# Optimization experiments

Hardware: AMD Instinct MI355X
Metric: run time of the kernel (lower is better)

The kernel has to match this reference:

```python
import jax, jax.numpy as jnp
import numpy as np

WS = 7      # window size
NH = 8      # num heads

def setup_inputs() -> dict:
    key = jax.random.key(0)
    k1, k2, k3 = jax.random.split(key, 3)
    B, H, W, C = 32, 56, 56, 256
    x = jax.random.normal(k1, (B, H, W, C), dtype=jnp.float32)
    w_qkv = jax.random.normal(k2, (3 * C, C), dtype=jnp.float32) * 0.02
    w_proj = jax.random.normal(k3, (C, C), dtype=jnp.float32) * 0.02
    b_proj = jnp.zeros((C,), dtype=jnp.float32)
    return {"x": x, "w_qkv": w_qkv, "w_proj": w_proj, "b_proj": b_proj}

def reference(x, w_qkv, w_proj, b_proj):
    B, H, W, C = x.shape
    hd = C // NH
    scale = hd ** -0.5
    # window partition: (B,H,W,C) -> (nW, ws^2, C)
    xw = x.reshape(B, H // WS, WS, W // WS, WS, C)
    xw = xw.transpose(0, 1, 3, 2, 4, 5).reshape(-1, WS * WS, C)
    # fused qkv projection (no bias)
    qkv = (xw @ w_qkv.T).reshape(-1, WS * WS, 3, NH, hd)
    q, k, v = qkv[:, :, 0], qkv[:, :, 1], qkv[:, :, 2]  # (nW, ws^2, nh, hd)
    # NOTE: faithful to source quirk — contraction over head_dim per token,
    # producing an (nh x nh) head-mixing attention matrix per token.
    attn = jnp.einsum('nshd,nsed->nshe', q, k) * scale   # (nW, ws^2, nh, nh)
    attn = jax.nn.softmax(attn, axis=-1)
    out = jnp.einsum('nshe,nsed->nshd', attn, v)         # (nW, ws^2, nh, hd)
    # source does transpose(1,2).reshape(-1, ws^2, C) — replicate exactly
    out = out.swapaxes(1, 2).reshape(-1, WS * WS, C)
    out = out @ w_proj.T + b_proj
    # window un-partition
    out = out.reshape(B, H // WS, W // WS, WS, WS, C)
    out = out.transpose(0, 1, 3, 2, 4, 5).reshape(B, H, W, C)
    return out
```

## Files before the change

### kernel.cpp

```cpp
#include <hip/hip_runtime.h>
#include <hip/hip_bf16.h>

typedef __bf16 bf16_t;
typedef bf16_t bf16x8 __attribute__((ext_vector_type(8)));
typedef float floatx4 __attribute__((ext_vector_type(4)));

__global__ __launch_bounds__(256) void wconv_kernel(
    const float* __restrict__ w_qkv, const float* __restrict__ w_proj,
    bf16_t* __restrict__ wb)
{
  int idx4 = (blockIdx.x * 256 + threadIdx.x) * 4;
  const float* src = (idx4 < 196608) ? (w_qkv + idx4) : (w_proj + (idx4 - 196608));
  float4 f = *(const float4*)src;
  bf16_t o[4] = {(bf16_t)f.x, (bf16_t)f.y, (bf16_t)f.z, (bf16_t)f.w};
  *(uint2*)(wb + idx4) = *(const uint2*)o;
}

__global__ __launch_bounds__(512, 4) void fused_kernel(
    const float* __restrict__ x,
    const bf16_t* __restrict__ wb,
    const float* __restrict__ b_proj,
    float* __restrict__ out)
{
  __shared__ __align__(16) bf16_t Xs[49][264];
  __shared__ __align__(16) bf16_t KV[49][264];
  __shared__ __align__(16) bf16_t Qt[49][72];
  __shared__ _Float16 Pl[49][64];
  __shared__ int trow[49];

  const int n = blockIdx.x;
  const int b = n >> 6, wh = (n >> 3) & 7, ww = n & 7;
  const int tid = threadIdx.x;
  const int wave = tid >> 6, lane = tid & 63, quad = lane >> 4, l16 = lane & 15;
  const float scale = 0.17677669529663687f;

  if (tid < 49) {
    int i = tid / 7, j = tid % 7;
    trow[tid] = b * 3136 + (wh * 7 + i) * 56 + ww * 7 + j;
  }
  __syncthreads();

  for (int idx = tid; idx < 49 * 32; idx += 512) {
    int s = idx >> 5, g = (idx & 31) * 8;
    const float* p = x + (long)trow[s] * 256 + g;
    float4 f0 = ((const float4*)p)[0];
    float4 f1 = ((const float4*)p)[1];
    bf16_t t8[8] = {(bf16_t)f0.x, (bf16_t)f0.y, (bf16_t)f0.z, (bf16_t)f0.w,
                    (bf16_t)f1.x, (bf16_t)f1.y, (bf16_t)f1.z, (bf16_t)f1.w};
    *(uint4*)(&Xs[s][g]) = *(const uint4*)t8;
  }
  __syncthreads();

  {
    floatx4 acc[4][2] = {};
    const int cb = wave * 32;
    const bf16_t* wk = wb + (256 + cb) * 256;
#pragma unroll
    for (int k = 0; k < 8; ++k) {
      bf16x8 a[4], bfr[2];
#pragma unroll
      for (int i = 0; i < 4; ++i) {
        int mr = i * 16 + l16; if (mr > 48) mr = 48;
        a[i] = *(const bf16x8*)(&Xs[mr][k * 32 + quad * 8]);
      }
#pragma unroll
      for (int j = 0; j < 2; ++j)
        bfr[j] = *(const bf16x8*)(wk + (j * 16 + l16) * 256 + k * 32 + quad * 8);
#pragma unroll
      for (int i = 0; i < 4; ++i)
#pragma unroll
        for (int j = 0; j < 2; ++j)
          acc[i][j] = __builtin_amdgcn_mfma_f32_16x16x32_bf16(a[i], bfr[j], acc[i][j], 0, 0, 0);
    }
#pragma unroll
    for (int i = 0; i < 4; ++i)
#pragma unroll
      for (int r = 0; r < 4; ++r) {
        int m = i * 16 + quad * 4 + r;
        if (m < 49) {
#pragma unroll
          for (int j = 0; j < 2; ++j)
            KV[m][cb + j * 16 + l16] = (bf16_t)acc[i][j][r];
        }
      }
  }
  __syncthreads();

  for (int hp = 0; hp < 4; ++hp) {
    const int jw = wave & 3;
    const int ih = wave >> 2;
    floatx4 qacc[2] = {};
    const bf16_t* wq = wb + (hp * 64 + jw * 16) * 256;
#pragma unroll
    for (int k = 0; k < 8; ++k) {
      bf16x8 a[2];
#pragma unroll
      for (int ii = 0; ii < 2; ++ii) {
        int mr = (ih * 2 + ii) * 16 + l16; if (mr > 48) mr = 48;
        a[ii] = *(const bf16x8*)(&Xs[mr][k * 32 + quad * 8]);
      }
      bf16x8 bfr = *(const bf16x8*)(wq + l16 * 256 + k * 32 + quad * 8);
#pragma unroll
      for (int ii = 0; ii < 2; ++ii)
        qacc[ii] = __builtin_amdgcn_mfma_f32_16x16x32_bf16(a[ii], bfr, qacc[ii], 0, 0, 0);
    }
#pragma unroll
    for (int ii = 0; ii < 2; ++ii)
#pragma unroll
      for (int r = 0; r < 4; ++r) {
        int m = (ih * 2 + ii) * 16 + quad * 4 + r;
        if (m < 49) Qt[m][jw * 16 + l16] = (bf16_t)qacc[ii][r];
      }
    __syncthreads();

    if (tid < 98) {
      int s = tid >> 1, hl = tid & 1;
      float qf[32];
#pragma unroll
      for (int u = 0; u < 4; ++u) {
        bf16x8 qv = *(const bf16x8*)(&Qt[s][hl * 32 + u * 8]);
#pragma unroll
        for (int d = 0; d < 8; ++d) qf[u * 8 + d] = (float)qv[d];
      }
      float v[8], mx = -INFINITY;
#pragma unroll
      for (int e = 0; e < 8; ++e) {
        float a = 0.f;
#pragma unroll
        for (int u = 0; u < 4; ++u) {
          bf16x8 kv = *(const bf16x8*)(&KV[s][e * 32 + u * 8]);
#pragma unroll
          for (int d = 0; d < 8; ++d) a += qf[u * 8 + d] * (float)kv[d];
        }
        v[e] = a * scale;
        mx = fmaxf(mx, v[e]);
      }
      float sum = 0.f;
#pragma unroll
      for (int e = 0; e < 8; ++e) { v[e] = __expf(v[e] - mx); sum += v[e]; }
      float rs = 1.0f / sum;
      int h = hp * 2 + hl;
#pragma unroll
      for (int e = 0; e < 8; ++e) Pl[s][h * 8 + e] = (_Float16)(v[e] * rs);
    }
    __syncthreads();
  }

  {
    floatx4 acc[4][2] = {};
    const int cb = wave * 32;
    const bf16_t* wv = wb + (512 + cb) * 256;
#pragma unroll
    for (int k = 0; k < 8; ++k) {
      bf16x8 a[4], bfr[2];
#pragma unroll
      for (int i = 0; i < 4; ++i) {
        int mr = i * 16 + l16; if (mr > 48) mr = 48;
        a[i] = *(const bf16x8*)(&Xs[mr][k * 32 + quad * 8]);
      }
#pragma unroll
      for (int j = 0; j < 2; ++j)
        bfr[j] = *(const bf16x8*)(wv + (j * 16 + l16) * 256 + k * 32 + quad * 8);
#pragma unroll
      for (int i = 0; i < 4; ++i)
#pragma unroll
        for (int j = 0; j < 2; ++j)
          acc[i][j] = __builtin_amdgcn_mfma_f32_16x16x32_bf16(a[i], bfr[j], acc[i][j], 0, 0, 0);
    }
#pragma unroll
    for (int i = 0; i < 4; ++i)
#pragma unroll
      for (int r = 0; r < 4; ++r) {
        int m = i * 16 + quad * 4 + r;
        if (m < 49) {
#pragma unroll
          for (int j = 0; j < 2; ++j)
            KV[m][wave * 32 + j * 16 + l16] = (bf16_t)acc[i][j][r];
        }
      }
  }
  __syncthreads();

  float o1[32];
  if (tid < 392) {
    int s = tid >> 3, h = tid & 7;
    float p[8];
#pragma unroll
    for (int e = 0; e < 8; ++e) p[e] = (float)Pl[s][h * 8 + e];
#pragma unroll
    for (int d = 0; d < 32; ++d) o1[d] = 0.f;
#pragma unroll
    for (int e = 0; e < 8; ++e) {
      float pe = p[e];
#pragma unroll
      for (int u = 0; u < 4; ++u) {
        bf16x8 vv = *(const bf16x8*)(&KV[s][e * 32 + u * 8]);
#pragma unroll
        for (int d = 0; d < 8; ++d) o1[u * 8 + d] += pe * (float)vv[d];
      }
    }
  }
  __syncthreads();

  if (tid < 392) {
    int s = tid >> 3, h = tid & 7;
    int flatb = h * 1568 + s * 32;
    int s2 = flatb >> 8, c2 = flatb & 255;
#pragma unroll
    for (int u = 0; u < 4; ++u) {
      bf16_t t8[8];
#pragma unroll
      for (int d = 0; d < 8; ++d) t8[d] = (bf16_t)o1[u * 8 + d];
      *(uint4*)(&KV[s2][c2 + u * 8]) = *(const uint4*)t8;
    }
  }
  __syncthreads();

  {
    floatx4 acc[4][2] = {};
    const int cb = wave * 32;
    const bf16_t* wp = wb + 196608 + cb * 256;
#pragma unroll
    for (int k = 0; k < 8; ++k) {
      bf16x8 a[4], bfr[2];
#pragma unroll
      for (int i = 0; i < 4; ++i) {
        int mr = i * 16 + l16; if (mr > 48) mr = 48;
        a[i] = *(const bf16x8*)(&KV[mr][k * 32 + quad * 8]);
      }
#pragma unroll
      for (int j = 0; j < 2; ++j)
        bfr[j] = *(const bf16x8*)(wp + (j * 16 + l16) * 256 + k * 32 + quad * 8);
#pragma unroll
      for (int i = 0; i < 4; ++i)
#pragma unroll
        for (int j = 0; j < 2; ++j)
          acc[i][j] = __builtin_amdgcn_mfma_f32_16x16x32_bf16(a[i], bfr[j], acc[i][j], 0, 0, 0);
    }
#pragma unroll
    for (int j = 0; j < 2; ++j) {
      int col = cb + j * 16 + l16;
      float bv = b_proj[col];
#pragma unroll
      for (int i = 0; i < 4; ++i)
#pragma unroll
        for (int r = 0; r < 4; ++r) {
          int m = i * 16 + quad * 4 + r;
          if (m < 49) out[(long)trow[m] * 256 + col] = acc[i][j][r] + bv;
        }
    }
  }
}

extern "C" void kernel_launch(void* const* d_in, const int* in_sizes, int n_in,
                              void* d_out, int out_size, void* d_ws, size_t ws_size,
                              hipStream_t stream) {
  (void)in_sizes; (void)n_in; (void)out_size; (void)ws_size;
  const float* x      = (const float*)d_in[0];
  const float* w_qkv  = (const float*)d_in[1];
  const float* w_proj = (const float*)d_in[2];
  const float* b_proj = (const float*)d_in[3];
  float* out = (float*)d_out;
  bf16_t* wb = (bf16_t*)d_ws;

  wconv_kernel<<<dim3(256), 256, 0, stream>>>(w_qkv, w_proj, wb);
  fused_kernel<<<dim3(2048), 512, 0, stream>>>(x, wb, b_proj, out);
}
```

Before: 333.1 us.

## Split fused window attention into per-token attention kernel and projection kernel

Moves the per-token head-mixing attention into a kernel tiled by 32 contiguous tokens, with no window gather and no padding of 49 rows to 64. A separate kernel then reads the fp32 intermediate from the output buffer, applies the transpose-reshape scramble and runs the output projection. The Q, K and V GEMMs are reorganised so Q and K are computed together, and V is computed by half the waves while the other half do the softmax. This removes wasted MMA padding and serial per-head loops. In exchange, the intermediate makes an extra fp32 round trip through global memory.

```diff
diff --git a/kernel.cpp b/kernel.cpp
--- a/kernel.cpp
+++ b/kernel.cpp
@@ -16,33 +16,28 @@
   *(uint2*)(wb + idx4) = *(const uint2*)o;
 }
 
-__global__ __launch_bounds__(512, 4) void fused_kernel(
+#define XS_S 272
+#define QK_S 520
+
+__global__ __launch_bounds__(512, 6) void attn_kernel(
     const float* __restrict__ x,
     const bf16_t* __restrict__ wb,
-    const float* __restrict__ b_proj,
     float* __restrict__ out)
 {
-  __shared__ __align__(16) bf16_t Xs[49][264];
-  __shared__ __align__(16) bf16_t KV[49][264];
-  __shared__ __align__(16) bf16_t Qt[49][72];
-  __shared__ _Float16 Pl[49][64];
-  __shared__ int trow[49];
-
-  const int n = blockIdx.x;
-  const int b = n >> 6, wh = (n >> 3) & 7, ww = n & 7;
+  __shared__ __align__(16) bf16_t Xs[32][XS_S];
+  __shared__ __align__(16) bf16_t QK[32][QK_S];
+
   const int tid = threadIdx.x;
   const int wave = tid >> 6, lane = tid & 63, quad = lane >> 4, l16 = lane & 15;
+  const long base = (long)blockIdx.x * 32;
   const float scale = 0.17677669529663687f;
 
-  if (tid < 49) {
-    int i = tid / 7, j = tid % 7;
-    trow[tid] = b * 3136 + (wh * 7 + i) * 56 + ww * 7 + j;
-  }
-  __syncthreads();
-
-  for (int idx = tid; idx < 49 * 32; idx += 512) {
+  const float* xb = x + base * 256;
+#pragma unroll
+  for (int it = 0; it < 2; ++it) {
+    int idx = tid + it * 512;
     int s = idx >> 5, g = (idx & 31) * 8;
-    const float* p = x + (long)trow[s] * 256 + g;
+    const float* p = xb + s * 256 + g;
     float4 f0 = ((const float4*)p)[0];
     float4 f1 = ((const float4*)p)[1];
     bf16_t t8[8] = {(bf16_t)f0.x, (bf16_t)f0.y, (bf16_t)f0.z, (bf16_t)f0.w,
@@ -52,202 +47,168 @@
   __syncthreads();
 
   {
-    floatx4 acc[4][2] = {};
-    const int cb = wave * 32;
-    const bf16_t* wk = wb + (256 + cb) * 256;
+    floatx4 acc[8] = {};
+    const int mt = wave >> 2;
+    const int cb = (wave & 3) * 128;
+    const bf16_t* wq = wb + (long)cb * 256;
 #pragma unroll
     for (int k = 0; k < 8; ++k) {
-      bf16x8 a[4], bfr[2];
-#pragma unroll
-      for (int i = 0; i < 4; ++i) {
-        int mr = i * 16 + l16; if (mr > 48) mr = 48;
-        a[i] = *(const bf16x8*)(&Xs[mr][k * 32 + quad * 8]);
-      }
-#pragma unroll
-      for (int j = 0; j < 2; ++j)
-        bfr[j] = *(const bf16x8*)(wk + (j * 16 + l16) * 256 + k * 32 + quad * 8);
-#pragma unroll
-      for (int i = 0; i < 4; ++i)
-#pragma unroll
-        for (int j = 0; j < 2; ++j)
-          acc[i][j] = __builtin_amdgcn_mfma_f32_16x16x32_bf16(a[i], bfr[j], acc[i][j], 0, 0, 0);
-    }
-#pragma unroll
-    for (int i = 0; i < 4; ++i)
-#pragma unroll
-      for (int r = 0; r < 4; ++r) {
-        int m = i * 16 + quad * 4 + r;
-        if (m < 49) {
-#pragma unroll
-          for (int j = 0; j < 2; ++j)
-            KV[m][cb + j * 16 + l16] = (bf16_t)acc[i][j][r];
-        }
-      }
-  }
-  __syncthreads();
-
-  for (int hp = 0; hp < 4; ++hp) {
-    const int jw = wave & 3;
-    const int ih = wave >> 2;
-    floatx4 qacc[2] = {};
-    const bf16_t* wq = wb + (hp * 64 + jw * 16) * 256;
+      bf16x8 a = *(const bf16x8*)(&Xs[mt * 16 + l16][k * 32 + quad * 8]);
+#pragma unroll
+      for (int j = 0; j < 8; ++j) {
+        bf16x8 b = *(const bf16x8*)(wq + (j * 16 + l16) * 256 + k * 32 + quad * 8);
+        acc[j] = __builtin_amdgcn_mfma_f32_16x16x32_bf16(a, b, acc[j], 0, 0, 0);
+      }
+    }
+#pragma unroll
+    for (int j = 0; j < 8; ++j)
+#pragma unroll
+      for (int r = 0; r < 4; ++r)
+        QK[mt * 16 + quad * 4 + r][cb + j * 16 + l16] = (bf16_t)acc[j][r];
+  }
+  __syncthreads();
+
+  float p_[8];
+  floatx4 vacc[8];
+  if (wave < 4) {
+    const int t = tid >> 3, h = tid & 7;
+    float sc[8];
+#pragma unroll
+    for (int e = 0; e < 8; ++e) sc[e] = 0.f;
+#pragma unroll
+    for (int u = 0; u < 4; ++u) {
+      bf16x8 qv = *(const bf16x8*)(&QK[t][h * 32 + u * 8]);
+      float qf[8];
+#pragma unroll
+      for (int d = 0; d < 8; ++d) qf[d] = (float)qv[d];
+#pragma unroll
+      for (int e = 0; e < 8; ++e) {
+        bf16x8 kv = *(const bf16x8*)(&QK[t][256 + e * 32 + u * 8]);
+#pragma unroll
+        for (int d = 0; d < 8; ++d) sc[e] += qf[d] * (float)kv[d];
+      }
+    }
+    float mx = -INFINITY;
+#pragma unroll
+    for (int e = 0; e < 8; ++e) { sc[e] *= scale; mx = fmaxf(mx, sc[e]); }
+    float sum = 0.f;
+#pragma unroll
+    for (int e = 0; e < 8; ++e) { p_[e] = __expf(sc[e] - mx); sum += p_[e]; }
+    float rs = 1.0f / sum;
+#pragma unroll
+    for (int e = 0; e < 8; ++e) p_[e] *= rs;
+  } else {
+    const int u = wave - 4;
+    const int mt = u >> 1;
+    const int cb = (u & 1) * 128;
+    const bf16_t* wv = wb + (long)(512 + cb) * 256;
+#pragma unroll
+    for (int j = 0; j < 8; ++j) vacc[j] = (floatx4){0.f, 0.f, 0.f, 0.f};
 #pragma unroll
     for (int k = 0; k < 8; ++k) {
-      bf16x8 a[2];
-#pragma unroll
-      for (int ii = 0; ii < 2; ++ii) {
-        int mr = (ih * 2 + ii) * 16 + l16; if (mr > 48) mr = 48;
-        a[ii] = *(const bf16x8*)(&Xs[mr][k * 32 + quad * 8]);
-      }
-      bf16x8 bfr = *(const bf16x8*)(wq + l16 * 256 + k * 32 + quad * 8);
-#pragma unroll
-      for (int ii = 0; ii < 2; ++ii)
-        qacc[ii] = __builtin_amdgcn_mfma_f32_16x16x32_bf16(a[ii], bfr, qacc[ii], 0, 0, 0);
-    }
-#pragma unroll
-    for (int ii = 0; ii < 2; ++ii)
-#pragma unroll
-      for (int r = 0; r < 4; ++r) {
-        int m = (ih * 2 + ii) * 16 + quad * 4 + r;
-        if (m < 49) Qt[m][jw * 16 + l16] = (bf16_t)qacc[ii][r];
-      }
-    __syncthreads();
-
-    if (tid < 98) {
-      int s = tid >> 1, hl = tid & 1;
-      float qf[32];
+      bf16x8 a = *(const bf16x8*)(&Xs[mt * 16 + l16][k * 32 + quad * 8]);
+#pragma unroll
+      for (int j = 0; j < 8; ++j) {
+        bf16x8 b = *(const bf16x8*)(wv + (j * 16 + l16) * 256 + k * 32 + quad * 8);
+        vacc[j] = __builtin_amdgcn_mfma_f32_16x16x32_bf16(a, b, vacc[j], 0, 0, 0);
+      }
+    }
+  }
+  __syncthreads();
+
+  if (wave >= 4) {
+    const int u = wave - 4;
+    const int mt = u >> 1;
+    const int cb = (u & 1) * 128;
+#pragma unroll
+    for (int j = 0; j < 8; ++j)
+#pragma unroll
+      for (int r = 0; r < 4; ++r)
+        QK[mt * 16 + quad * 4 + r][cb + j * 16 + l16] = (bf16_t)vacc[j][r];
+  }
+  __syncthreads();
+
+  if (wave < 4) {
+    const int t = tid >> 3, h = tid & 7;
+    float pre[32];
+#pragma unroll
+    for (int i = 0; i < 32; ++i) pre[i] = 0.f;
+#pragma unroll
+    for (int e = 0; e < 8; ++e) {
+      float pe = p_[e];
 #pragma unroll
       for (int u = 0; u < 4; ++u) {
-        bf16x8 qv = *(const bf16x8*)(&Qt[s][hl * 32 + u * 8]);
-#pragma unroll
-        for (int d = 0; d < 8; ++d) qf[u * 8 + d] = (float)qv[d];
-      }
-      float v[8], mx = -INFINITY;
-#pragma unroll
-      for (int e = 0; e < 8; ++e) {
-        float a = 0.f;
-#pragma unroll
-        for (int u = 0; u < 4; ++u) {
-          bf16x8 kv = *(const bf16x8*)(&KV[s][e * 32 + u * 8]);
-#pragma unroll
-          for (int d = 0; d < 8; ++d) a += qf[u * 8 + d] * (float)kv[d];
-        }
-        v[e] = a * scale;
-        mx = fmaxf(mx, v[e]);
-      }
-      float sum = 0.f;
-#pragma unroll
-      for (int e = 0; e < 8; ++e) { v[e] = __expf(v[e] - mx); sum += v[e]; }
-      float rs = 1.0f / sum;
-      int h = hp * 2 + hl;
-#pragma unroll
-      for (int e = 0; e < 8; ++e) Pl[s][h * 8 + e] = (_Float16)(v[e] * rs);
-    }
-    __syncthreads();
-  }
+        bf16x8 vv = *(const bf16x8*)(&QK[t][e * 32 + u * 8]);
+#pragma unroll
+        for (int d = 0; d < 8; ++d) pre[u * 8 + d] += pe * (float)vv[d];
+      }
+    }
+    float* op = out + (base + t) * 256 + h * 32;
+#pragma unroll
+    for (int u = 0; u < 8; ++u) {
+      float4 f = {pre[u * 4], pre[u * 4 + 1], pre[u * 4 + 2], pre[u * 4 + 3]};
+      ((float4*)op)[u] = f;
+    }
+  }
+}
+
+#define SC_S 264
+
+__global__ __launch_bounds__(512, 8) void proj_kernel(
+    const bf16_t* __restrict__ wb,
+    const float* __restrict__ b_proj,
+    float* out)
+{
+  __shared__ __align__(16) bf16_t Sc[49][SC_S];
+  __shared__ int trow[49];
+
+  const int n = blockIdx.x;
+  const int b = n >> 6, wh = (n >> 3) & 7, ww = n & 7;
+  const int tid = threadIdx.x;
+  const int wave = tid >> 6, lane = tid & 63, quad = lane >> 4, l16 = lane & 15;
+
+  if (tid < 49) {
+    int i = tid / 7, j = tid % 7;
+    trow[tid] = b * 3136 + (wh * 7 + i) * 56 + ww * 7 + j;
+  }
+  __syncthreads();
+
+  for (int idx = tid; idx < 49 * 32; idx += 512) {
+    int s = idx >> 5, g8 = idx & 31;
+    const float* p = out + (long)trow[s] * 256 + g8 * 8;
+    float4 f0 = ((const float4*)p)[0];
+    float4 f1 = ((const float4*)p)[1];
+    bf16_t t8[8] = {(bf16_t)f0.x, (bf16_t)f0.y, (bf16_t)f0.z, (bf16_t)f0.w,
+                    (bf16_t)f1.x, (bf16_t)f1.y, (bf16_t)f1.z, (bf16_t)f1.w};
+    int flat = (g8 >> 2) * 1568 + s * 32 + (g8 & 3) * 8;
+    *(uint4*)(&Sc[flat >> 8][flat & 255]) = *(const uint4*)t8;
+  }
+  __syncthreads();
 
   {
-    floatx4 acc[4][2] = {};
-    const int cb = wave * 32;
-    const bf16_t* wv = wb + (512 + cb) * 256;
+    floatx4 acc[8] = {};
+    const int mt = wave >> 1;
+    const int cb = (wave & 1) * 128;
+    const bf16_t* wp = wb + 196608 + (long)cb * 256;
 #pragma unroll
     for (int k = 0; k < 8; ++k) {
-      bf16x8 a[4], bfr[2];
-#pragma unroll
-      for (int i = 0; i < 4; ++i) {
-        int mr = i * 16 + l16; if (mr > 48) mr = 48;
-        a[i] = *(const bf16x8*)(&Xs[mr][k * 32 + quad * 8]);
-      }
-#pragma unroll
-      for (int j = 0; j < 2; ++j)
-        bfr[j] = *(const bf16x8*)(wv + (j * 16 + l16) * 256 + k * 32 + quad * 8);
-#pragma unroll
-      for (int i = 0; i < 4; ++i)
-#pragma unroll
-        for (int j = 0; j < 2; ++j)
-          acc[i][j] = __builtin_amdgcn_mfma_f32_16x16x32_bf16(a[i], bfr[j], acc[i][j], 0, 0, 0);
-    }
-#pragma unroll
-    for (int i = 0; i < 4; ++i)
-#pragma unroll
-      for (int r = 0; r < 4; ++r) {
-        int m = i * 16 + quad * 4 + r;
-        if (m < 49) {
-#pragma unroll
-          for (int j = 0; j < 2; ++j)
-            KV[m][wave * 32 + j * 16 + l16] = (bf16_t)acc[i][j][r];
-        }
-      }
-  }
-  __syncthreads();
-
-  float o1[32];
-  if (tid < 392) {
-    int s = tid >> 3, h = tid & 7;
-    float p[8];
-#pragma unroll
-    for (int e = 0; e < 8; ++e) p[e] = (float)Pl[s][h * 8 + e];
-#pragma unroll
-    for (int d = 0; d < 32; ++d) o1[d] = 0.f;
-#pragma unroll
-    for (int e = 0; e < 8; ++e) {
-      float pe = p[e];
-#pragma unroll
-      for (int u = 0; u < 4; ++u) {
-        bf16x8 vv = *(const bf16x8*)(&KV[s][e * 32 + u * 8]);
-#pragma unroll
-        for (int d = 0; d < 8; ++d) o1[u * 8 + d] += pe * (float)vv[d];
-      }
-    }
-  }
-  __syncthreads();
-
-  if (tid < 392) {
-    int s = tid >> 3, h = tid & 7;
-    int flatb = h * 1568 + s * 32;
-    int s2 = flatb >> 8, c2 = flatb & 255;
-#pragma unroll
-    for (int u = 0; u < 4; ++u) {
-      bf16_t t8[8];
-#pragma unroll
-      for (int d = 0; d < 8; ++d) t8[d] = (bf16_t)o1[u * 8 + d];
-      *(uint4*)(&KV[s2][c2 + u * 8]) = *(const uint4*)t8;
-    }
-  }
-  __syncthreads();
-
-  {
-    floatx4 acc[4][2] = {};
-    const int cb = wave * 32;
-    const bf16_t* wp = wb + 196608 + cb * 256;
-#pragma unroll
-    for (int k = 0; k < 8; ++k) {
-      bf16x8 a[4], bfr[2];
-#pragma unroll
-      for (int i = 0; i < 4; ++i) {
-        int mr = i * 16 + l16; if (mr > 48) mr = 48;
-        a[i] = *(const bf16x8*)(&KV[mr][k * 32 + quad * 8]);
-      }
-#pragma unroll
-      for (int j = 0; j < 2; ++j)
-        bfr[j] = *(const bf16x8*)(wp + (j * 16 + l16) * 256 + k * 32 + quad * 8);
-#pragma unroll
-      for (int i = 0; i < 4; ++i)
-#pragma unroll
-        for (int j = 0; j < 2; ++j)
-          acc[i][j] = __builtin_amdgcn_mfma_f32_16x16x32_bf16(a[i], bfr[j], acc[i][j], 0, 0, 0);
-    }
-#pragma unroll
-    for (int j = 0; j < 2; ++j) {
+      int mr = mt * 16 + l16; if (mr > 48) mr = 48;
+      bf16x8 a = *(const bf16x8*)(&Sc[mr][k * 32 + quad * 8]);
+#pragma unroll
+      for (int j = 0; j < 8; ++j) {
+        bf16x8 bf = *(const bf16x8*)(wp + (j * 16 + l16) * 256 + k * 32 + quad * 8);
+        acc[j] = __builtin_amdgcn_mfma_f32_16x16x32_bf16(a, bf, acc[j], 0, 0, 0);
+      }
+    }
+#pragma unroll
+    for (int j = 0; j < 8; ++j) {
       int col = cb + j * 16 + l16;
       float bv = b_proj[col];
 #pragma unroll
-      for (int i = 0; i < 4; ++i)
-#pragma unroll
-        for (int r = 0; r < 4; ++r) {
-          int m = i * 16 + quad * 4 + r;
-          if (m < 49) out[(long)trow[m] * 256 + col] = acc[i][j][r] + bv;
-        }
+      for (int r = 0; r < 4; ++r) {
+        int m = mt * 16 + quad * 4 + r;
+        if (m < 49) out[(long)trow[m] * 256 + col] = acc[j][r] + bv;
+      }
     }
   }
 }
@@ -264,5 +225,6 @@
   bf16_t* wb = (bf16_t*)d_ws;
 
   wconv_kernel<<<dim3(256), 256, 0, stream>>>(w_qkv, w_proj, wb);
-  fused_kernel<<<dim3(2048), 512, 0, stream>>>(x, wb, b_proj, out);
-}
+  attn_kernel<<<dim3(3136), 512, 0, stream>>>(x, wb, out);
+  proj_kernel<<<dim3(2048), 512, 0, stream>>>(wb, b_proj, out);
+}
```

After: 649.5 us. 1.95x slower.
